# Optimization experiments

Measured on AMD Instinct MI355X. Metric: run time of the kernel, lower is better.

## Reference

```python
import jax, jax.numpy as jnp
import numpy as np

WIDTH_POW = 10
WIDTH = 2 ** WIDTH_POW          # 1024
HALF = WIDTH // 2               # 512
DEPTH = 32
BATCH = 32768


def setup_inputs() -> dict:
    key = jax.random.key(0)
    kx, ks, kr = jax.random.split(key, 3)
    X = jax.random.normal(kx, (BATCH, WIDTH), dtype=jnp.float32)
    # Replicate the torch init: rand_sgn * (1 - rand/depth) / 2 + 0.5
    rand_sgn = (jax.random.randint(ks, (HALF, DEPTH), 0, 2) * 2 - 1).astype(jnp.float32)
    u = jax.random.uniform(kr, (HALF, DEPTH), dtype=jnp.float32)
    params = rand_sgn * (1.0 - u / DEPTH) / 2.0 + 0.5
    return {"X": X, "params": params}


def reference(X, params):
    """Doubly stochastic butterfly: at each depth step, each feature pair
    (j, j+half) is mixed by the 2x2 doubly stochastic block [[1-w, w], [w, 1-w]]
    with w = params[j, i]. Vectorized over batch; depth handled by lax.scan."""
    half = params.shape[0]

    def step(x, w):
        # x: [B, 2*half], w: [half]
        x0 = x[:, :half]
        x1 = x[:, half:]
        new_x0 = x0 * (1.0 - w) + x1 * w
        new_x1 = x1 * (1.0 - w) + x0 * w
        return jnp.concatenate([new_x0, new_x1], axis=1), None

    out, _ = jax.lax.scan(step, X, params.T)  # scan over depth axis
    return out
```

## Files before the change

kernel.cpp:

```cpp
#include <hip/hip_runtime.h>

#define WIDTH  1024
#define HALF   512
#define DEPTH  32
#define BATCH  32768
#define PAIRS4 (HALF / 4)
#define NTHREADS 256
#define NBLOCKS  2048

typedef float f4 __attribute__((ext_vector_type(4)));

__global__ void __launch_bounds__(NTHREADS)
butterfly_fused(const float* __restrict__ X,
                const float* __restrict__ params,
                float* __restrict__ out) {
    __shared__ float gs[HALF];

    const int tid = threadIdx.x;

    for (int j = tid; j < HALF; j += NTHREADS) {
        const float* p = params + j * DEPTH;
        float prod = 1.0f;
#pragma unroll
        for (int i = 0; i < DEPTH; ++i) {
            prod *= (1.0f - 2.0f * p[i]);
        }
        gs[j] = prod;
    }
    __syncthreads();

    const long long total = (long long)BATCH * PAIRS4;
    const long long stride = (long long)NBLOCKS * NTHREADS;

    for (long long idx = (long long)blockIdx.x * NTHREADS + tid;
         idx < total; idx += stride) {
        const int b  = (int)(idx >> 7);
        const int jv = (int)(idx & 127);

        const f4* x0p = (const f4*)(X + (long long)b * WIDTH);
        const f4* x1p = x0p + PAIRS4;

        f4 x0 = __builtin_nontemporal_load(x0p + jv);
        f4 x1 = __builtin_nontemporal_load(x1p + jv);
        f4 gv = ((const f4*)gs)[jv];

        f4 h = 0.5f * (x0 + x1);
        f4 e = 0.5f * (x0 - x1) * gv;
        f4 o0 = h + e;
        f4 o1 = h - e;

        f4* o0p = (f4*)(out + (long long)b * WIDTH);
        f4* o1p = o0p + PAIRS4;
        __builtin_nontemporal_store(o0, o0p + jv);
        __builtin_nontemporal_store(o1, o1p + jv);
    }
}

extern "C" void kernel_launch(void* const* d_in, const int* in_sizes, int n_in,
                              void* d_out, int out_size, void* d_ws, size_t ws_size,
                              hipStream_t stream) {
    const float* X      = (const float*)d_in[0];
    const float* params = (const float*)d_in[1];
    float* out = (float*)d_out;

    hipLaunchKernelGGL(butterfly_fused, dim3(NBLOCKS), dim3(NTHREADS), 0, stream,
                       X, params, out);
}
```

Before: 229.4 us.

## Compute per-thread gains in registers and overlap with first row load

Removes the shared-memory gain table and block barrier; each thread computes the four gain products for its own columns straight from params, while the first row's X load is already in flight. Each thread then processes eight rows strided through the batch, replacing the grid-stride loop with a fixed unrolled loop. The cost is redundant param reads across threads, which are cached but add load traffic.

```diff
diff --git a/kernel.cpp b/kernel.cpp
--- a/kernel.cpp
+++ b/kernel.cpp
@@ -7,6 +7,8 @@
 #define PAIRS4 (HALF / 4)
 #define NTHREADS 256
 #define NBLOCKS  2048
+#define ROWS_PER_THREAD 8
+#define ROW_STRIDE 4096
 
 typedef float f4 __attribute__((ext_vector_type(4)));
 
@@ -14,45 +16,45 @@
 butterfly_fused(const float* __restrict__ X,
                 const float* __restrict__ params,
                 float* __restrict__ out) {
-    __shared__ float gs[HALF];
+    const int tid0  = blockIdx.x * NTHREADS + threadIdx.x;
+    const int jv    = tid0 & (PAIRS4 - 1);
+    const int brow0 = tid0 >> 7;
 
-    const int tid = threadIdx.x;
+    const float* xbase = X   + (long long)brow0 * WIDTH + 4 * jv;
+    float*       obase = out + (long long)brow0 * WIDTH + 4 * jv;
 
-    for (int j = tid; j < HALF; j += NTHREADS) {
-        const float* p = params + j * DEPTH;
-        float prod = 1.0f;
+    f4 x0_0 = __builtin_nontemporal_load((const f4*)(xbase));
+    f4 x1_0 = __builtin_nontemporal_load((const f4*)(xbase + HALF));
+
+    f4 g2;
 #pragma unroll
-        for (int i = 0; i < DEPTH; ++i) {
-            prod *= (1.0f - 2.0f * p[i]);
+    for (int r = 0; r < 4; ++r) {
+        const f4* prow = (const f4*)(params + (4 * jv + r) * DEPTH);
+        f4 prod = {1.0f, 1.0f, 1.0f, 1.0f};
+#pragma unroll
+        for (int c = 0; c < DEPTH / 4; ++c) {
+            f4 p = prow[c];
+            prod *= (1.0f - 2.0f * p);
         }
-        gs[j] = prod;
+        g2[r] = 0.5f * (prod.x * prod.y * prod.z * prod.w);
     }
-    __syncthreads();
 
-    const long long total = (long long)BATCH * PAIRS4;
-    const long long stride = (long long)NBLOCKS * NTHREADS;
+    {
+        f4 h = 0.5f * (x0_0 + x1_0);
+        f4 e = (x0_0 - x1_0) * g2;
+        __builtin_nontemporal_store(h + e, (f4*)(obase));
+        __builtin_nontemporal_store(h - e, (f4*)(obase + HALF));
+    }
 
-    for (long long idx = (long long)blockIdx.x * NTHREADS + tid;
-         idx < total; idx += stride) {
-        const int b  = (int)(idx >> 7);
-        const int jv = (int)(idx & 127);
-
-        const f4* x0p = (const f4*)(X + (long long)b * WIDTH);
-        const f4* x1p = x0p + PAIRS4;
-
-        f4 x0 = __builtin_nontemporal_load(x0p + jv);
-        f4 x1 = __builtin_nontemporal_load(x1p + jv);
-        f4 gv = ((const f4*)gs)[jv];
-
+#pragma unroll
+    for (int k = 1; k < ROWS_PER_THREAD; ++k) {
+        const long long off = (long long)k * ROW_STRIDE * WIDTH;
+        f4 x0 = __builtin_nontemporal_load((const f4*)(xbase + off));
+        f4 x1 = __builtin_nontemporal_load((const f4*)(xbase + off + HALF));
         f4 h = 0.5f * (x0 + x1);
-        f4 e = 0.5f * (x0 - x1) * gv;
-        f4 o0 = h + e;
-        f4 o1 = h - e;
-
-        f4* o0p = (f4*)(out + (long long)b * WIDTH);
-        f4* o1p = o0p + PAIRS4;
-        __builtin_nontemporal_store(o0, o0p + jv);
-        __builtin_nontemporal_store(o1, o1p + jv);
+        f4 e = (x0 - x1) * g2;
+        __builtin_nontemporal_store(h + e, (f4*)(obase + off));
+        __builtin_nontemporal_store(h - e, (f4*)(obase + off + HALF));
     }
 }
 
```

New measurement: 239.5 us. 1.04x slower.
